# Optimization experiments

Measured on AMD Instinct MI355X. Metric: run time of the kernel, lower is better.

The kernel has to match this reference:

```python
import jax, jax.numpy as jnp
import numpy as np

B, S, H = 1, 1024, 2048
NH, NKV, HD = 32, 4, 128
E, K, I = 32, 8, 768
EPS = 1e-06
ROPE_BASE = 1e6


def rmsnorm(x, w, eps=EPS):
    xf = x.astype(jnp.float32)
    var = jnp.mean(xf * xf, axis=-1, keepdims=True)
    return w * (xf * jax.lax.rsqrt(var + eps)).astype(x.dtype)


def apply_rope(x, cos, sin):
    # x: [B,S,N,HD]; cos/sin: [S,HD//2]; interleaved (llama-style) pair rotation
    xr = x.reshape(*x.shape[:-1], HD // 2, 2)
    x0, x1 = xr[..., 0], xr[..., 1]
    c = cos[None, :, None, :]
    s = sin[None, :, None, :]
    o0 = x0 * c - x1 * s
    o1 = x0 * s + x1 * c
    return jnp.stack([o0, o1], axis=-1).reshape(x.shape)


def setup_inputs() -> dict:
    key = jax.random.key(0)
    ks = jax.random.split(key, 16)
    hidden_states = jax.random.normal(ks[0], (B, S, H), dtype=jnp.float32)
    # RoPE angles: positions * inv_freq  -> [S, HD//2]
    inv_freq = 1.0 / (ROPE_BASE ** (np.arange(0, HD, 2, dtype=np.float32) / HD))
    position_embeddings = jnp.asarray(np.arange(S, dtype=np.float32)[:, None] * inv_freq[None, :])
    # causal additive mask [1,1,S,S]
    causal = jnp.tril(jnp.ones((S, S), dtype=bool))
    attention_mask = jnp.where(causal, 0.0, -1e9).astype(jnp.float32)[None, None]
    w = 0.02
    params = {
        'ln1_w': jnp.ones((H,), jnp.float32),
        'ln2_w': jnp.ones((H,), jnp.float32),
        'q_w': w * jax.random.normal(ks[1], (H, NH * HD), jnp.float32),
        'k_w': w * jax.random.normal(ks[2], (H, NKV * HD), jnp.float32),
        'v_w': w * jax.random.normal(ks[3], (H, NKV * HD), jnp.float32),
        'o_w': w * jax.random.normal(ks[4], (NH * HD, H), jnp.float32),
        'qn_w': jnp.ones((HD,), jnp.float32),
        'kn_w': jnp.ones((HD,), jnp.float32),
        'gate_w': w * jax.random.normal(ks[5], (H, E), jnp.float32),
        'wg': w * jax.random.normal(ks[6], (E, H, I), jnp.float32),
        'wu': w * jax.random.normal(ks[7], (E, H, I), jnp.float32),
        'wd': w * jax.random.normal(ks[8], (E, I, H), jnp.float32),
    }
    return {'hidden_states': hidden_states, 'position_embeddings': position_embeddings,
            'attention_mask': attention_mask, 'start_pos': 0, **params}


def reference(hidden_states, position_embeddings, attention_mask, start_pos,
              ln1_w, ln2_w, q_w, k_w, v_w, o_w, qn_w, kn_w, gate_w, wg, wu, wd):
    x = hidden_states  # [B,S,H]
    # --- attention ---
    h = rmsnorm(x, ln1_w)
    q = rmsnorm((h @ q_w).reshape(B, S, NH, HD), qn_w)
    k = rmsnorm((h @ k_w).reshape(B, S, NKV, HD), kn_w)
    v = (h @ v_w).reshape(B, S, NKV, HD)
    cos, sin = jnp.cos(position_embeddings), jnp.sin(position_embeddings)
    q = apply_rope(q, cos, sin)
    k = apply_rope(k, cos, sin)
    q = q.transpose(0, 2, 1, 3)  # [B,NH,S,HD]
    k = jnp.repeat(k.transpose(0, 2, 1, 3), NH // NKV, axis=1)
    v = jnp.repeat(v.transpose(0, 2, 1, 3), NH // NKV, axis=1)
    scores = jnp.einsum('bhqd,bhkd->bhqk', q, k) * (HD ** -0.5) + attention_mask
    attn = jax.nn.softmax(scores, axis=-1)
    o = jnp.einsum('bhqk,bhkd->bhqd', attn, v).transpose(0, 2, 1, 3).reshape(B, S, NH * HD)
    x = x + o @ o_w
    # --- MoE ---
    h = rmsnorm(x, ln2_w).reshape(B * S, H)  # [T,H]
    probs = jax.nn.softmax((h @ gate_w).astype(jnp.float32), axis=-1)
    rw, sel = jax.lax.top_k(probs, K)  # [T,K]
    rw = rw / jnp.sum(rw, axis=-1, keepdims=True)  # norm_topk_prob
    T = B * S
    # dense combine weights [T,E]; zero for unselected experts (same math as loop)
    wte = jnp.zeros((T, E), jnp.float32).at[jnp.arange(T)[:, None], sel].add(rw).astype(h.dtype)
    g = jnp.einsum('th,ehi->tei', h, wg)
    u = jnp.einsum('th,ehi->tei', h, wu)
    act = jax.nn.silu(g) * u  # [T,E,I]
    moe = jnp.einsum('te,tei,eih->th', wte, act, wd)
    return x + moe.reshape(B, S, H)
```

## Files before the change

### kernel.cpp

```cpp
#include <hip/hip_runtime.h>
#include <hip/hip_bf16.h>

#define S_ 1024
#define H_ 2048
#define NH_ 32
#define NKV_ 4
#define HD_ 128
#define NE_ 32
#define TOPK_ 8
#define I_ 768
#define EPS_ 1e-6f
#define QS_ 5120
#define BK2 32
#define NPAR 4

typedef __bf16 bf16_t;
typedef __bf16 bf16x4v __attribute__((ext_vector_type(4)));
typedef __bf16 bf16x8 __attribute__((ext_vector_type(8)));
typedef float f32x4 __attribute__((ext_vector_type(4)));
typedef float f32x16 __attribute__((ext_vector_type(16)));
typedef unsigned short u16_t;
typedef unsigned int uint2v __attribute__((ext_vector_type(2)));
typedef unsigned int uint4v __attribute__((ext_vector_type(4)));

static __device__ __forceinline__ u16_t f2u(float x) {
  return __builtin_bit_cast(u16_t, (__bf16)x);
}
static __device__ __forceinline__ float u2f(u16_t u) {
  return (float)__builtin_bit_cast(__bf16, u);
}

static __device__ __forceinline__ void gload16(const bf16_t* g, bf16_t* l) {
  __builtin_amdgcn_global_load_lds(
      (const __attribute__((address_space(1))) unsigned int*)g,
      (__attribute__((address_space(3))) unsigned int*)l, 16, 0, 0);
}

static __device__ __forceinline__ int tile_lane_off(int lane) {
  return (lane >> 2) * 32 + (((lane & 3) ^ ((lane >> 3) & 3)) << 3);
}

template <bool WF32>
__global__ __launch_bounds__(256) void rmsnorm2_k(const float* __restrict__ x,
                                                  const float* __restrict__ w,
                                                  float* __restrict__ outf,
                                                  bf16_t* __restrict__ outb) {
  int r = blockIdx.x, tid = threadIdx.x;
  const float* xr = x + (size_t)r * H_;
  f32x4 a = *(const f32x4*)(xr + tid * 8);
  f32x4 b = *(const f32x4*)(xr + tid * 8 + 4);
  float ss = 0.f;
#pragma unroll
  for (int i = 0; i < 4; ++i) ss += a[i] * a[i] + b[i] * b[i];
#pragma unroll
  for (int m = 1; m < 64; m <<= 1) ss += __shfl_xor(ss, m);
  __shared__ float wsum[4];
  if ((tid & 63) == 0) wsum[tid >> 6] = ss;
  __syncthreads();
  ss = wsum[0] + wsum[1] + wsum[2] + wsum[3];
  float inv = rsqrtf(ss * (1.0f / H_) + EPS_);
  f32x4 w0 = *(const f32x4*)(w + tid * 8);
  f32x4 w1 = *(const f32x4*)(w + tid * 8 + 4);
  f32x4 o0, o1;
#pragma unroll
  for (int i = 0; i < 4; ++i) { o0[i] = a[i] * inv * w0[i]; o1[i] = b[i] * inv * w1[i]; }
  if constexpr (WF32) {
    *(f32x4*)(outf + (size_t)r * H_ + tid * 8) = o0;
    *(f32x4*)(outf + (size_t)r * H_ + tid * 8 + 4) = o1;
  }
  bf16x8 ob;
#pragma unroll
  for (int i = 0; i < 4; ++i) { ob[i] = (__bf16)o0[i]; ob[i + 4] = (__bf16)o1[i]; }
  *(bf16x8*)(outb + (size_t)r * H_ + tid * 8) = ob;
}

__global__ __launch_bounds__(256) void transp3_k(const float* __restrict__ in,
                                                 bf16_t* __restrict__ out, int R, int C) {
  __shared__ float tile[64][65];
  size_t z = (size_t)blockIdx.z * R * C;
  int tx = threadIdx.x & 15, ty = threadIdx.x >> 4;
  int r0 = blockIdx.y * 64, c0 = blockIdx.x * 64;
#pragma unroll
  for (int i = 0; i < 4; ++i) {
    f32x4 v = *(const f32x4*)(in + z + (size_t)(r0 + ty + i * 16) * C + c0 + tx * 4);
    tile[ty + i * 16][tx * 4 + 0] = v[0];
    tile[ty + i * 16][tx * 4 + 1] = v[1];
    tile[ty + i * 16][tx * 4 + 2] = v[2];
    tile[ty + i * 16][tx * 4 + 3] = v[3];
  }
  __syncthreads();
  int KT = R >> 5;
  int flat = threadIdx.x * 16;
  int lt = flat >> 9;
  int within = flat & 511;
  int nr = within >> 5;
  int kc = within & 31;
  int tn = lt >> 1, tk = lt & 1;
  bf16x8 o0, o1;
#pragma unroll
  for (int j = 0; j < 8; ++j) o0[j] = (bf16_t)tile[tk * 32 + kc + j][tn * 16 + nr];
#pragma unroll
  for (int j = 0; j < 8; ++j) o1[j] = (bf16_t)tile[tk * 32 + kc + 8 + j][tn * 16 + nr];
  size_t tidx = ((size_t)((c0 >> 4) + tn) * KT + (r0 >> 5) + tk) << 9;
  *(bf16x8*)(out + z + tidx + nr * 32 + kc) = o0;
  *(bf16x8*)(out + z + tidx + nr * 32 + kc + 8) = o1;
}

template <int BMT, int BNT, int WM, int WN, typename TC, bool RESID>
__global__ __launch_bounds__(512) void gemmd_k(
    const bf16_t* __restrict__ A, const bf16_t* __restrict__ Bt,
    const float* __restrict__ resid, TC* __restrict__ C, int M, int N, int K) {
  constexpr int MI = BMT / WM / 16;
  constexpr int NI = BNT / WN / 16;
  constexpr int ALW = BMT / 16 / 8;
  constexpr int NBL = BNT / 16;
  static_assert(NBL <= 8, "B wave loads");
  __shared__ __align__(16) bf16_t As[2][BMT][BK2];
  __shared__ __align__(16) bf16_t Bs[2][BNT][BK2];
  int tid = threadIdx.x, lane = tid & 63, w = tid >> 6;
  int m0 = blockIdx.x * BMT, n0 = blockIdx.y * BNT;
  int srow = lane >> 2;
  int schunk = ((lane & 3) ^ ((lane >> 3) & 3)) * 8;
  const bf16_t* asrc[ALW];
#pragma unroll
  for (int i = 0; i < ALW; ++i) {
    int r = (w * ALW + i) * 16 + srow;
    asrc[i] = A + (size_t)(m0 + r) * K + schunk;
  }
  bool hasB = (w < NBL);
  int brow = w * 16;
  const bf16_t* bsrc = nullptr;
  if (hasB)
    bsrc = Bt + ((size_t)((n0 + brow) >> 4) * (K >> 5)) * 512 + tile_lane_off(lane);

  int fr = lane & 15, g = lane >> 4;
  int rk = (g ^ ((fr >> 1) & 3)) * 8;
  int wm = w / WN, wn = w % WN;
  int rbase0 = wm * (BMT / WM), cbase0 = wn * (BNT / WN);
  f32x4 acc[MI][NI] = {};
  int NT = K / BK2;
  {
#pragma unroll
    for (int i = 0; i < ALW; ++i) gload16(asrc[i], &As[0][(w * ALW + i) * 16][0]);
    if (hasB) gload16(bsrc, &Bs[0][brow][0]);
  }
  __syncthreads();
  int cur = 0;
  for (int t = 0; t < NT; ++t) {
    if (t + 1 < NT) {
      int ko = (t + 1) * BK2;
#pragma unroll
      for (int i = 0; i < ALW; ++i) gload16(asrc[i] + ko, &As[cur ^ 1][(w * ALW + i) * 16][0]);
      if (hasB) gload16(bsrc + (size_t)(t + 1) * 512, &Bs[cur ^ 1][brow][0]);
    }
    bf16x8 af[MI], bf[NI];
#pragma unroll
    for (int i = 0; i < MI; ++i) af[i] = *(const bf16x8*)&As[cur][rbase0 + i * 16 + fr][rk];
#pragma unroll
    for (int i = 0; i < NI; ++i) bf[i] = *(const bf16x8*)&Bs[cur][cbase0 + i * 16 + fr][rk];
#pragma unroll
    for (int mi = 0; mi < MI; ++mi)
#pragma unroll
      for (int ni = 0; ni < NI; ++ni)
        acc[mi][ni] = __builtin_amdgcn_mfma_f32_16x16x32_bf16(af[mi], bf[ni], acc[mi][ni], 0, 0, 0);
    __syncthreads();
    cur ^= 1;
  }
  int rbase = g * 4;
#pragma unroll
  for (int mi = 0; mi < MI; ++mi)
#pragma unroll
    for (int ni = 0; ni < NI; ++ni)
#pragma unroll
      for (int r = 0; r < 4; ++r) {
        int gi = m0 + rbase0 + mi * 16 + rbase + r;
        int gc = n0 + cbase0 + ni * 16 + fr;
        float v = acc[mi][ni][r];
        if constexpr (RESID) v += resid[(size_t)gi * N + gc];
        C[(size_t)gi * N + gc] = (TC)v;
      }
}

template <int BNT, int WM, int WN, typename TC, bool GATHER, bool SCALE, bool DUAL>
__global__ __launch_bounds__(512) void gemme2_k(
    const bf16_t* __restrict__ A, const bf16_t* __restrict__ B1g,
    const bf16_t* __restrict__ B2g, TC* __restrict__ C, bf16_t* __restrict__ act,
    const float* __restrict__ wlist, const int* __restrict__ counts,
    const int* __restrict__ offsets, const int* __restrict__ toklist,
    const int* __restrict__ mslots, const int* __restrict__ meta,
    int* __restrict__ qhead, int NTN, int N, int K) {
  constexpr int BMT = 128;
  constexpr int MI = BMT / WM / 16;
  constexpr int NI = BNT / WN / 16;
  constexpr int BNTT = BNT * (DUAL ? 2 : 1);
  constexpr int NBT = BNTT / 16;
  constexpr int BPW = NBT / 8;
  static_assert(BPW * 8 == NBT, "B tile split");
  __shared__ __align__(16) bf16_t As[4][BMT][BK2];
  __shared__ __align__(16) bf16_t Bs[4][BNTT][BK2];
  __shared__ int s_w;
  int tid = threadIdx.x, lane = tid & 63, w = tid >> 6;
  int srow = lane >> 2;
  int schunk = ((lane & 3) ^ ((lane >> 3) & 3)) * 8;
  int tloff = tile_lane_off(lane);
  int fr = lane & 15, g = lane >> 4;
  int rk = (g ^ ((fr >> 1) & 3)) * 8;
  int wm = w / WN, wn = w % WN;
  int rbase0 = wm * (BMT / WM), cbase0 = wn * (BNT / WN);
  int KT = K >> 5;
  int SS = K >> 7;
  int total = meta[0] * NTN;
  for (;;) {
    if (tid == 0) s_w = atomicAdd(qhead, 1);
    __syncthreads();
    int wk = s_w;
    if (wk >= total) return;
    int ms = mslots[wk / NTN];
    int n0 = (wk % NTN) * BNT;
    int e = ms >> 8, m0 = (ms & 255) * BMT;
    int cnt = counts[e], off = offsets[e];
    size_t bs = (size_t)K * N;
    const bf16_t* B1 = B1g + (size_t)e * bs;
    const bf16_t* B2 = DUAL ? (B2g + (size_t)e * bs) : nullptr;
    const bf16_t* asrc;
    {
      int gr = min(m0 + w * 16 + srow, cnt - 1);
      size_t grow;
      if constexpr (GATHER) grow = (size_t)toklist[e * S_ + gr];
      else grow = (size_t)(off + gr);
      asrc = A + grow * (size_t)K + schunk;
    }
    const bf16_t* bsrc[BPW];
    int brow16[BPW];
#pragma unroll
    for (int j = 0; j < BPW; ++j) {
      int r16 = (w * BPW + j) * 16;
      brow16[j] = r16;
      const bf16_t* Bb = (r16 < BNT) ? B1 : B2;
      int rr = (r16 < BNT) ? r16 : r16 - BNT;
      bsrc[j] = Bb + ((size_t)((n0 + rr) >> 4) * KT) * 512 + tloff;
    }
    f32x4 acc1[MI][NI] = {};
    f32x4 acc2[DUAL ? MI : 1][DUAL ? NI : 1] = {};
    for (int ss = 0; ss < SS; ++ss) {
      int kbase = ss * 128;
#pragma unroll
      for (int sub = 0; sub < 4; ++sub)
        gload16(asrc + kbase + sub * BK2, &As[sub][w * 16][0]);
#pragma unroll
      for (int j = 0; j < BPW; ++j)
#pragma unroll
        for (int sub = 0; sub < 4; ++sub)
          gload16(bsrc[j] + (size_t)(ss * 4 + sub) * 512, &Bs[sub][brow16[j]][0]);
      __syncthreads();
#pragma unroll
      for (int sub = 0; sub < 4; ++sub) {
        bf16x8 af[MI], b1f[NI], b2f[DUAL ? NI : 1];
#pragma unroll
        for (int i = 0; i < MI; ++i) af[i] = *(const bf16x8*)&As[sub][rbase0 + i * 16 + fr][rk];
#pragma unroll
        for (int i = 0; i < NI; ++i) b1f[i] = *(const bf16x8*)&Bs[sub][cbase0 + i * 16 + fr][rk];
        if constexpr (DUAL) {
#pragma unroll
          for (int i = 0; i < NI; ++i) b2f[i] = *(const bf16x8*)&Bs[sub][BNT + cbase0 + i * 16 + fr][rk];
        }
#pragma unroll
        for (int mi = 0; mi < MI; ++mi)
#pragma unroll
          for (int ni = 0; ni < NI; ++ni) {
            acc1[mi][ni] = __builtin_amdgcn_mfma_f32_16x16x32_bf16(af[mi], b1f[ni], acc1[mi][ni], 0, 0, 0);
            if constexpr (DUAL)
              acc2[mi][ni] = __builtin_amdgcn_mfma_f32_16x16x32_bf16(af[mi], b2f[ni], acc2[mi][ni], 0, 0, 0);
          }
      }
      __syncthreads();
    }
    int rbase = g * 4;
#pragma unroll
    for (int mi = 0; mi < MI; ++mi)
#pragma unroll
      for (int ni = 0; ni < NI; ++ni)
#pragma unroll
        for (int r = 0; r < 4; ++r) {
          int lr = rbase0 + mi * 16 + rbase + r;
          int gi = m0 + lr;
          if (gi >= cnt) continue;
          int gc = n0 + cbase0 + ni * 16 + fr;
          if constexpr (DUAL) {
            float gv = acc1[mi][ni][r], uv = acc2[mi][ni][r];
            float sig = 1.0f / (1.0f + __expf(-gv));
            act[(size_t)(off + gi) * N + gc] = (bf16_t)(gv * sig * uv);
          } else {
            float v = acc1[mi][ni][r];
            if constexpr (SCALE) v *= wlist[(size_t)e * S_ + gi];
            C[(size_t)(off + gi) * N + gc] = (TC)v;
          }
        }
  }
}

__global__ __launch_bounds__(64) void qkpack_k(const float* __restrict__ qkv,
                                               const float* __restrict__ qn,
                                               const float* __restrict__ kn,
                                               const float* __restrict__ pe,
                                               bf16_t* __restrict__ Q2,
                                               bf16_t* __restrict__ K2) {
  int s = blockIdx.x, hh = blockIdx.y, lane = threadIdx.x;
  const float* ptr;
  const float* w;
  if (hh < NH_) { ptr = qkv + (size_t)s * QS_ + hh * HD_; w = qn; }
  else          { ptr = qkv + (size_t)s * QS_ + NH_ * HD_ + (hh - NH_) * HD_; w = kn; }
  float x0 = ptr[2 * lane], x1 = ptr[2 * lane + 1];
  float ss = x0 * x0 + x1 * x1;
#pragma unroll
  for (int m = 1; m < 64; m <<= 1) ss += __shfl_xor(ss, m);
  float inv = rsqrtf(ss * (1.0f / HD_) + EPS_);
  x0 = x0 * inv * w[2 * lane];
  x1 = x1 * inv * w[2 * lane + 1];
  float ang = pe[(size_t)s * (HD_ / 2) + lane];
  float sn, cs;
  sincosf(ang, &sn, &cs);
  float r0 = x0 * cs - x1 * sn;
  float r1 = x0 * sn + x1 * cs;
  if (hh < NH_) {
    const float scale = 0.08838834764831845f;
    float a = r0 * scale, b = r1 * scale;
    u16_t h0 = f2u(a), h1 = f2u(b);
    unsigned hw = (unsigned)h0 | ((unsigned)h1 << 16);
    unsigned lw = (unsigned)f2u(a - u2f(h0)) | ((unsigned)f2u(b - u2f(h1)) << 16);
    unsigned* base = (unsigned*)(Q2 + ((size_t)s * NH_ + hh) * 256);
    base[lane] = hw;
    base[64 + lane] = lw;
  } else {
    u16_t h0 = f2u(r0), h1 = f2u(r1);
    unsigned hw = (unsigned)h0 | ((unsigned)h1 << 16);
    unsigned lw = (unsigned)f2u(r0 - u2f(h0)) | ((unsigned)f2u(r1 - u2f(h1)) << 16);
    int j = lane >> 2, off = (2 * lane) & 7;
    unsigned* base = (unsigned*)(K2 + ((size_t)(hh - NH_) * S_ + s) * 256);
    base[(((j) ^ (s & 31)) * 8 + off) >> 1] = hw;
    base[(((16 + j) ^ (s & 31)) * 8 + off) >> 1] = lw;
  }
}

__global__ __launch_bounds__(256) void vpack_k(const float* __restrict__ qkv,
                                               bf16_t* __restrict__ V2T) {
  int t = blockIdx.x, kvh = blockIdx.y;
  int kv0 = t * 64;
  bf16_t* dst = V2T + (size_t)(kvh * 16 + t) * 128 * 128;
  const float* vbase = qkv + NH_ * HD_ + NKV_ * HD_ + kvh * HD_;
#pragma unroll
  for (int i = 0; i < 4; ++i) {
    int flat = threadIdx.x + i * 256;
    int kvp = flat >> 5, d4 = (flat & 31) * 4;
    const float* r0 = vbase + (size_t)(kv0 + 2 * kvp) * QS_ + d4;
    const float* r1 = r0 + QS_;
    f32x4 a = *(const f32x4*)r0;
    f32x4 b = *(const f32x4*)r1;
    int kvg = (2 * kvp) >> 3, sub = (2 * kvp) & 7;
#pragma unroll
    for (int e = 0; e < 4; ++e) {
      int d = d4 + e;
      int fsw = (d ^ (d >> 4)) & 15;
      u16_t ha = f2u(a[e]), hb = f2u(b[e]);
      unsigned hw = (unsigned)ha | ((unsigned)hb << 16);
      unsigned lw = (unsigned)f2u(a[e] - u2f(ha)) | ((unsigned)f2u(b[e] - u2f(hb)) << 16);
      unsigned* dd = (unsigned*)(dst + d * 128);
      dd[((kvg ^ fsw) * 8 + sub) >> 1] = hw;
      dd[(((8 + kvg) ^ fsw) * 8 + sub) >> 1] = lw;
    }
  }
}

#define AKV 64
__global__ __launch_bounds__(512, 4) void attn5_k(const bf16_t* __restrict__ Q2,
                                                  const bf16_t* __restrict__ K2,
                                                  const bf16_t* __restrict__ V2T,
                                                  float* __restrict__ Op,
                                                  float* __restrict__ mlp) {
  int q0 = blockIdx.x * 32;
  int kvh = blockIdx.y;
  int par = blockIdx.z;
  int tid = threadIdx.x, lane = tid & 63, w = tid >> 6;
  int g = lane >> 5, c32 = lane & 31;
  int h = kvh * 8 + w;
  int qrow = q0 + c32;
  int last_t = (q0 + 31) >> 6;
  float2* mlv = (float2*)mlp;
  if (par > last_t) {
    if (g == 0) {
      float2 v2; v2.x = -3.0e38f; v2.y = 0.f;
      mlv[((size_t)par * S_ + qrow) * NH_ + h] = v2;
    }
    return;
  }
  __shared__ __align__(16) u16_t Kl[AKV * 256];
  __shared__ __align__(16) u16_t Vl[128 * 128];

  bf16x8 qh[8], ql[8];
  {
    const bf16_t* qp2 = Q2 + ((size_t)qrow * NH_ + h) * 256;
#pragma unroll
    for (int ks = 0; ks < 8; ++ks) {
      qh[ks] = *(const bf16x8*)(qp2 + g * 8 + ks * 16);
      ql[ks] = *(const bf16x8*)(qp2 + 128 + g * 8 + ks * 16);
    }
  }

  f32x16 accO[4] = {};
  float m = -3.0e38f, l = 0.f;

  for (int t = par; t <= last_t; t += NPAR) {
    int kv0 = t * AKV;
    __syncthreads();
    {
      const bf16_t* ksrc = K2 + ((size_t)kvh * S_ + kv0) * 256;
#pragma unroll
      for (int i = 0; i < 4; ++i) {
        int cbase = w * 64 + i * 512;
        gload16(ksrc + (size_t)(cbase + lane) * 8, (bf16_t*)&Kl[cbase * 8]);
      }
    }
    {
      const bf16_t* vsrc = V2T + (size_t)(kvh * 16 + t) * 128 * 128;
#pragma unroll
      for (int i = 0; i < 4; ++i) {
        int cbase = w * 64 + i * 512;
        gload16(vsrc + (size_t)(cbase + lane) * 8, (bf16_t*)&Vl[cbase * 8]);
      }
    }
    __syncthreads();

    f32x16 accS[2] = {};
#pragma unroll
    for (int ks = 0; ks < 8; ++ks) {
      int db = g * 8 + ks * 16;
#pragma unroll
      for (int mf = 0; mf < 2; ++mf) {
        int kvr = c32 + mf * 32;
        bf16x8 ah = *(const bf16x8*)&Kl[kvr * 256 + (((db >> 3)) ^ c32) * 8];
        bf16x8 al = *(const bf16x8*)&Kl[kvr * 256 + ((16 + (db >> 3)) ^ c32) * 8];
        accS[mf] = __builtin_amdgcn_mfma_f32_32x32x16_bf16(ah, qh[ks], accS[mf], 0, 0, 0);
        accS[mf] = __builtin_amdgcn_mfma_f32_32x32x16_bf16(ah, ql[ks], accS[mf], 0, 0, 0);
        accS[mf] = __builtin_amdgcn_mfma_f32_32x32x16_bf16(al, qh[ks], accS[mf], 0, 0, 0);
      }
    }
    float p[2][16];
    float tmax = -3.0e38f;
#pragma unroll
    for (int mf = 0; mf < 2; ++mf)
#pragma unroll
      for (int r = 0; r < 16; ++r) {
        int kvg = kv0 + mf * 32 + (r & 3) + 8 * (r >> 2) + 4 * g;
        float s = (kvg <= qrow) ? accS[mf][r] : -3.0e38f;
        p[mf][r] = s;
        tmax = fmaxf(tmax, s);
      }
    tmax = fmaxf(tmax, __shfl_xor(tmax, 32));
    float mn = fmaxf(m, tmax);
    float sc = __expf(m - mn);
    float ts = 0.f;
#pragma unroll
    for (int mf = 0; mf < 2; ++mf)
#pragma unroll
      for (int r = 0; r < 16; ++r) {
        float e = __expf(p[mf][r] - mn);
        p[mf][r] = e;
        ts += e;
      }
    ts += __shfl_xor(ts, 32);
    l = l * sc + ts;
    m = mn;
#pragma unroll
    for (int r = 0; r < 16; ++r) {
      int row16 = (r & 3) + 8 * (r >> 2) + 4 * g;
      float scr = __shfl(sc, row16);
#pragma unroll
      for (int nf = 0; nf < 4; ++nf) accO[nf][r] *= scr;
    }
#pragma unroll
    for (int ks = 0; ks < 4; ++ks) {
      int k1 = ks & 1, mf = ks >> 1;
      unsigned Lh[4], Ll[4];
#pragma unroll
      for (int i = 0; i < 4; ++i) {
        float a = p[mf][8 * k1 + 2 * i], b = p[mf][8 * k1 + 2 * i + 1];
        u16_t ha = f2u(a), hb = f2u(b);
        Lh[i] = (unsigned)ha | ((unsigned)hb << 16);
        Ll[i] = (unsigned)f2u(a - u2f(ha)) | ((unsigned)f2u(b - u2f(hb)) << 16);
      }
      unsigned Xh[4], Xl[4];
#pragma unroll
      for (int i = 0; i < 4; ++i) {
        Xh[i] = (unsigned)__shfl_xor((int)Lh[i], 32);
        Xl[i] = (unsigned)__shfl_xor((int)Ll[i], 32);
      }
      uint4v fh, fl;
      fh[0] = g ? Xh[2] : Lh[0]; fh[1] = g ? Xh[3] : Lh[1];
      fh[2] = g ? Lh[2] : Xh[0]; fh[3] = g ? Lh[3] : Xh[1];
      fl[0] = g ? Xl[2] : Ll[0]; fl[1] = g ? Xl[3] : Ll[1];
      fl[2] = g ? Ll[2] : Xl[0]; fl[3] = g ? Ll[3] : Xl[1];
      bf16x8 pH = __builtin_bit_cast(bf16x8, fh);
      bf16x8 pL = __builtin_bit_cast(bf16x8, fl);
      int kvb = g * 8 + ks * 16;
#pragma unroll
      for (int nf = 0; nf < 4; ++nf) {
        int d = c32 + nf * 32;
        int fsw = (d ^ (d >> 4)) & 15;
        bf16x8 vh = *(const bf16x8*)&Vl[d * 128 + (((kvb >> 3)) ^ fsw) * 8];
        bf16x8 vl = *(const bf16x8*)&Vl[d * 128 + ((8 + (kvb >> 3)) ^ fsw) * 8];
        accO[nf] = __builtin_amdgcn_mfma_f32_32x32x16_bf16(pH, vh, accO[nf], 0, 0, 0);
        accO[nf] = __builtin_amdgcn_mfma_f32_32x32x16_bf16(pH, vl, accO[nf], 0, 0, 0);
        accO[nf] = __builtin_amdgcn_mfma_f32_32x32x16_bf16(pL, vh, accO[nf], 0, 0, 0);
      }
    }
  }
#pragma unroll
  for (int r = 0; r < 16; ++r) {
    int row16 = (r & 3) + 8 * (r >> 2) + 4 * g;
    int orow = q0 + row16;
#pragma unroll
    for (int nf = 0; nf < 4; ++nf)
      __builtin_nontemporal_store(
          accO[nf][r], &Op[(((size_t)par * S_ + orow) * NH_ + h) * HD_ + nf * 32 + c32]);
  }
  if (g == 0) {
    float2 v2; v2.x = m; v2.y = l;
    mlv[((size_t)par * S_ + qrow) * NH_ + h] = v2;
  }
}

__global__ __launch_bounds__(128) void attnmerge_k(const float* __restrict__ Op,
                                                   const float* __restrict__ mlp,
                                                   bf16_t* __restrict__ o) {
  int row = blockIdx.x, h = blockIdx.y, d = threadIdx.x;
  const float2* mlv = (const float2*)mlp;
  float mm[NPAR], ll[NPAR];
  float M = -3.0e38f;
#pragma unroll
  for (int p = 0; p < NPAR; ++p) {
    float2 v2 = mlv[((size_t)p * S_ + row) * NH_ + h];
    mm[p] = v2.x; ll[p] = v2.y;
    M = fmaxf(M, mm[p]);
  }
  float acc = 0.f, L = 0.f;
#pragma unroll
  for (int p = 0; p < NPAR; ++p) {
    if (ll[p] == 0.f) continue;
    float wp = __expf(mm[p] - M);
    acc += wp * __builtin_nontemporal_load(
                    &Op[(((size_t)p * S_ + row) * NH_ + h) * HD_ + d]);
    L += wp * ll[p];
  }
  o[((size_t)row * NH_ + h) * HD_ + d] = (bf16_t)(acc / L);
}

__global__ __launch_bounds__(256) void router2_k(const float* __restrict__ h2,
                                                 const float* __restrict__ gw,
                                                 int* __restrict__ sel,
                                                 float* __restrict__ wsel) {
  int t = blockIdx.x, tid = threadIdx.x;
  int e = tid & 31, grp = tid >> 5;
  float acc = 0.f;
  for (int kk = grp; kk < H_; kk += 8)
    acc += h2[(size_t)t * H_ + kk] * gw[(size_t)kk * NE_ + e];
  __shared__ float part[8][32];
  part[grp][e] = acc;
  __syncthreads();
  if (tid < 64) {
    int lane = tid;
    float lg = -3.0e38f;
    if (lane < 32) {
      lg = 0.f;
      for (int g = 0; g < 8; ++g) lg += part[g][lane];
    }
    float tm = lg;
#pragma unroll
    for (int mm = 1; mm < 32; mm <<= 1) tm = fmaxf(tm, __shfl_xor(tm, mm));
    if (lane < 32) lg = __expf(lg - tm);
    bool avail = (lane < 32);
    float tot = 0.f;
    int se[TOPK_]; float rw[TOPK_];
#pragma unroll
    for (int kk = 0; kk < TOPK_; ++kk) {
      float val = avail ? lg : -1.f;
      float best = val;
#pragma unroll
      for (int mm = 1; mm < 32; mm <<= 1) best = fmaxf(best, __shfl_xor(best, mm));
      unsigned long long ball = __ballot(avail && (val == best));
      int bi = (int)__builtin_ctzll(ball);
      if (lane == bi) avail = false;
      se[kk] = bi;
      rw[kk] = best;
      tot += best;
    }
    float itot = 1.0f / tot;
    if (lane == 0) {
#pragma unroll
      for (int kk = 0; kk < TOPK_; ++kk) {
        sel[t * TOPK_ + kk] = se[kk];
        wsel[t * TOPK_ + kk] = rw[kk] * itot;
      }
    }
  }
}

__global__ __launch_bounds__(64) void build_k(const int* __restrict__ sel,
                                              const float* __restrict__ wsel,
                                              int* __restrict__ counts,
                                              int* __restrict__ toklist,
                                              float* __restrict__ wlist,
                                              int* __restrict__ pos) {
  int e = blockIdx.x, lane = threadIdx.x;
  int base = 0;
  for (int c = 0; c < S_ / 64; ++c) {
    int t = c * 64 + lane;
    int match = -1;
#pragma unroll
    for (int k = 0; k < TOPK_; ++k)
      if (sel[t * TOPK_ + k] == e) match = k;
    bool flag = (match >= 0);
    unsigned long long mask = __ballot(flag);
    int prefix = __popcll(mask & ((1ull << lane) - 1ull));
    if (flag) {
      int p = base + prefix;
      toklist[e * S_ + p] = t;
      wlist[e * S_ + p] = wsel[t * TOPK_ + match];
      pos[t * TOPK_ + match] = p;
    }
    base += __popcll(mask);
  }
  if (lane == 0) counts[e] = base;
}

__global__ void scan_k(const int* __restrict__ counts, int* __restrict__ offsets,
                       int* __restrict__ mslots, int* __restrict__ meta,
                       int* __restrict__ qheads) {
  if (threadIdx.x == 0 && blockIdx.x == 0) {
    int o = 0, ns = 0;
    for (int e = 0; e < NE_; ++e) {
      offsets[e] = o;
      int c = counts[e];
      for (int m0 = 0; m0 < c; m0 += 128) mslots[ns++] = (e << 8) | (m0 >> 7);
      o += c;
    }
    offsets[NE_] = o;
    meta[0] = ns;
    qheads[0] = 0;
    qheads[1] = 0;
  }
}

__global__ __launch_bounds__(256) void combine_k(const float* __restrict__ x1,
                                                 const bf16_t* __restrict__ pairout,
                                                 const int* __restrict__ sel,
                                                 const int* __restrict__ pos,
                                                 const int* __restrict__ offsets,
                                                 float* __restrict__ out) {
  int t = blockIdx.x, tid = threadIdx.x;
  int slots[TOPK_];
#pragma unroll
  for (int kk = 0; kk < TOPK_; ++kk)
    slots[kk] = offsets[sel[t * TOPK_ + kk]] + pos[t * TOPK_ + kk];
  int c = tid * 8;
  f32x4 s0 = *(const f32x4*)(x1 + (size_t)t * H_ + c);
  f32x4 s1 = *(const f32x4*)(x1 + (size_t)t * H_ + c + 4);
#pragma unroll
  for (int kk = 0; kk < TOPK_; ++kk) {
    bf16x8 pv = *(const bf16x8*)(pairout + (size_t)slots[kk] * H_ + c);
#pragma unroll
    for (int i = 0; i < 4; ++i) { s0[i] += (float)pv[i]; s1[i] += (float)pv[i + 4]; }
  }
  *(f32x4*)(out + (size_t)t * H_ + c) = s0;
  *(f32x4*)(out + (size_t)t * H_ + c + 4) = s1;
}

extern "C" void kernel_launch(void* const* d_in, const int* in_sizes, int n_in,
                              void* d_out, int out_size, void* d_ws, size_t ws_size,
                              hipStream_t stream) {
  const float* hidden = (const float*)d_in[0];
  const float* pe     = (const float*)d_in[1];
  const float* ln1    = (const float*)d_in[4];
  const float* ln2    = (const float*)d_in[5];
  const float* q_w    = (const float*)d_in[6];
  const float* k_w    = (const float*)d_in[7];
  const float* v_w    = (const float*)d_in[8];
  const float* o_w    = (const float*)d_in[9];
  const float* qn     = (const float*)d_in[10];
  const float* kn     = (const float*)d_in[11];
  const float* gate_w = (const float*)d_in[12];
  const float* wg     = (const float*)d_in[13];
  const float* wu     = (const float*)d_in[14];
  const float* wd     = (const float*)d_in[15];
  float* out = (float*)d_out;

  char* p = (char*)d_ws;
  auto alloc = [&](size_t bytes) {
    char* r = p;
    p += (bytes + 255) & ~(size_t)255;
    return r;
  };
  bf16_t* h1b     = (bf16_t*)alloc((size_t)S_ * H_ * 2);
  float*  qkv     = (float*)alloc((size_t)S_ * QS_ * 4);
  bf16_t* Q2      = (bf16_t*)alloc((size_t)S_ * NH_ * 256 * 2);
  bf16_t* K2      = (bf16_t*)alloc((size_t)NKV_ * S_ * 256 * 2);
  bf16_t* V2T     = (bf16_t*)alloc((size_t)NKV_ * 16 * 128 * 128 * 2);
  bf16_t* aob     = (bf16_t*)alloc((size_t)S_ * NH_ * HD_ * 2);
  float*  x1      = (float*)alloc((size_t)S_ * H_ * 4);
  float*  h2      = (float*)alloc((size_t)S_ * H_ * 4);
  bf16_t* h2b     = (bf16_t*)alloc((size_t)S_ * H_ * 2);
  bf16_t* act     = (bf16_t*)alloc((size_t)S_ * TOPK_ * I_ * 2);
  bf16_t* po      = (bf16_t*)alloc((size_t)S_ * TOPK_ * H_ * 2);
  float*  Opart   = (float*)alloc((size_t)NPAR * S_ * NH_ * HD_ * 4);
  float*  mlpart  = (float*)alloc((size_t)NPAR * S_ * NH_ * 8);
  int*    counts  = (int*)alloc(NE_ * 4);
  int*    offs    = (int*)alloc((NE_ + 1) * 4);
  int*    toklist = (int*)alloc((size_t)NE_ * S_ * 4);
  float*  wlist   = (float*)alloc((size_t)NE_ * S_ * 4);
  int*    sel     = (int*)alloc((size_t)S_ * TOPK_ * 4);
  float*  wsel    = (float*)alloc((size_t)S_ * TOPK_ * 4);
  int*    pos     = (int*)alloc((size_t)S_ * TOPK_ * 4);
  int*    mslots  = (int*)alloc(512 * 4);
  int*    meta    = (int*)alloc(4);
  int*    qheads  = (int*)alloc(2 * 4);
  bf16_t* qkvT = (bf16_t*)alloc((size_t)QS_ * H_ * 2);
  bf16_t* owT  = (bf16_t*)alloc((size_t)(NH_ * HD_) * H_ * 2);
  bf16_t* wgT  = (bf16_t*)alloc((size_t)NE_ * H_ * I_ * 2);
  bf16_t* wuT  = (bf16_t*)alloc((size_t)NE_ * H_ * I_ * 2);
  bf16_t* wdT  = (bf16_t*)alloc((size_t)NE_ * I_ * H_ * 2);
  bf16_t* qwTp = qkvT;
  bf16_t* kwTp = qkvT + (size_t)(NH_ * HD_) * H_;
  bf16_t* vwTp = qkvT + (size_t)(NH_ * HD_ + NKV_ * HD_) * H_;

  transp3_k<<<dim3((NH_ * HD_) / 64, H_ / 64, 1), 256, 0, stream>>>(q_w, qwTp, H_, NH_ * HD_);
  transp3_k<<<dim3((NKV_ * HD_) / 64, H_ / 64, 1), 256, 0, stream>>>(k_w, kwTp, H_, NKV_ * HD_);
  transp3_k<<<dim3((NKV_ * HD_) / 64, H_ / 64, 1), 256, 0, stream>>>(v_w, vwTp, H_, NKV_ * HD_);
  transp3_k<<<dim3(H_ / 64, (NH_ * HD_) / 64, 1), 256, 0, stream>>>(o_w, owT, NH_ * HD_, H_);
  transp3_k<<<dim3(I_ / 64, H_ / 64, NE_), 256, 0, stream>>>(wg, wgT, H_, I_);
  transp3_k<<<dim3(I_ / 64, H_ / 64, NE_), 256, 0, stream>>>(wu, wuT, H_, I_);
  transp3_k<<<dim3(H_ / 64, I_ / 64, NE_), 256, 0, stream>>>(wd, wdT, I_, H_);

  rmsnorm2_k<false><<<S_, 256, 0, stream>>>(hidden, ln1, nullptr, h1b);
  gemmd_k<256, 128, 4, 2, float, false>
      <<<dim3(S_ / 256, QS_ / 128), 512, 0, stream>>>(h1b, qkvT, nullptr, qkv, S_, QS_, H_);
  qkpack_k<<<dim3(S_, NH_ + NKV_), 64, 0, stream>>>(qkv, qn, kn, pe, Q2, K2);
  vpack_k<<<dim3(16, NKV_), 256, 0, stream>>>(qkv, V2T);
  attn5_k<<<dim3(S_ / 32, NKV_, NPAR), 512, 0, stream>>>(Q2, K2, V2T, Opart, mlpart);
  attnmerge_k<<<dim3(S_, NH_), 128, 0, stream>>>(Opart, mlpart, aob);
  gemmd_k<128, 64, 4, 2, float, true>
      <<<dim3(S_ / 128, H_ / 64), 512, 0, stream>>>(aob, owT, hidden, x1, S_, H_, NH_ * HD_);
  rmsnorm2_k<true><<<S_, 256, 0, stream>>>(x1, ln2, h2, h2b);
  router2_k<<<S_, 256, 0, stream>>>(h2, gate_w, sel, wsel);
  build_k<<<NE_, 64, 0, stream>>>(sel, wsel, counts, toklist, wlist, pos);
  scan_k<<<1, 64, 0, stream>>>(counts, offs, mslots, meta, qheads);
  gemme2_k<128, 2, 4, float, true, false, true>
      <<<256, 512, 0, stream>>>(h2b, wgT, wuT, nullptr, act, wlist, counts, offs, toklist,
                                mslots, meta, &qheads[0], I_ / 128, I_, H_);
  gemme2_k<256, 2, 4, bf16_t, false, true, false>
      <<<256, 512, 0, stream>>>(act, wdT, nullptr, po, nullptr, wlist, counts, offs, nullptr,
                                mslots, meta, &qheads[1], H_ / 256, H_, I_);
  combine_k<<<S_, 256, 0, stream>>>(x1, po, sel, pos, offs, out);
}
```

Baseline: 830.2 us.

## Drop split-KV attention and merge kernel; normalize output in-kernel

Removes the 4-way KV split of the attention kernel and the separate merge kernel. Each block now walks all causal KV tiles itself, divides by the softmax sum in registers and writes bf16 output directly. This saves the fp32 partial-output round trip through memory and one kernel launch. In exchange the grid shrinks fourfold (128 blocks), so there is less parallelism and the causal work is spread less evenly across blocks.

```diff
diff --git a/kernel.cpp b/kernel.cpp
--- a/kernel.cpp
+++ b/kernel.cpp
@@ -12,7 +12,6 @@
 #define EPS_ 1e-6f
 #define QS_ 5120
 #define BK2 32
-#define NPAR 4
 
 typedef __bf16 bf16_t;
 typedef __bf16 bf16x4v __attribute__((ext_vector_type(4)));
@@ -372,27 +371,17 @@
 }
 
 #define AKV 64
-__global__ __launch_bounds__(512, 4) void attn5_k(const bf16_t* __restrict__ Q2,
+__global__ __launch_bounds__(512, 2) void attn6_k(const bf16_t* __restrict__ Q2,
                                                   const bf16_t* __restrict__ K2,
                                                   const bf16_t* __restrict__ V2T,
-                                                  float* __restrict__ Op,
-                                                  float* __restrict__ mlp) {
+                                                  bf16_t* __restrict__ o) {
   int q0 = blockIdx.x * 32;
   int kvh = blockIdx.y;
-  int par = blockIdx.z;
   int tid = threadIdx.x, lane = tid & 63, w = tid >> 6;
   int g = lane >> 5, c32 = lane & 31;
   int h = kvh * 8 + w;
   int qrow = q0 + c32;
   int last_t = (q0 + 31) >> 6;
-  float2* mlv = (float2*)mlp;
-  if (par > last_t) {
-    if (g == 0) {
-      float2 v2; v2.x = -3.0e38f; v2.y = 0.f;
-      mlv[((size_t)par * S_ + qrow) * NH_ + h] = v2;
-    }
-    return;
-  }
   __shared__ __align__(16) u16_t Kl[AKV * 256];
   __shared__ __align__(16) u16_t Vl[128 * 128];
 
@@ -409,7 +398,7 @@
   f32x16 accO[4] = {};
   float m = -3.0e38f, l = 0.f;
 
-  for (int t = par; t <= last_t; t += NPAR) {
+  for (int t = 0; t <= last_t; ++t) {
     int kv0 = t * AKV;
     __syncthreads();
     {
@@ -514,44 +503,16 @@
       }
     }
   }
+  float invl = 1.0f / l;
 #pragma unroll
   for (int r = 0; r < 16; ++r) {
     int row16 = (r & 3) + 8 * (r >> 2) + 4 * g;
+    float il = __shfl(invl, row16);
     int orow = q0 + row16;
 #pragma unroll
     for (int nf = 0; nf < 4; ++nf)
-      __builtin_nontemporal_store(
-          accO[nf][r], &Op[(((size_t)par * S_ + orow) * NH_ + h) * HD_ + nf * 32 + c32]);
-  }
-  if (g == 0) {
-    float2 v2; v2.x = m; v2.y = l;
-    mlv[((size_t)par * S_ + qrow) * NH_ + h] = v2;
-  }
-}
-
-__global__ __launch_bounds__(128) void attnmerge_k(const float* __restrict__ Op,
-                                                   const float* __restrict__ mlp,
-                                                   bf16_t* __restrict__ o) {
-  int row = blockIdx.x, h = blockIdx.y, d = threadIdx.x;
-  const float2* mlv = (const float2*)mlp;
-  float mm[NPAR], ll[NPAR];
-  float M = -3.0e38f;
-#pragma unroll
-  for (int p = 0; p < NPAR; ++p) {
-    float2 v2 = mlv[((size_t)p * S_ + row) * NH_ + h];
-    mm[p] = v2.x; ll[p] = v2.y;
-    M = fmaxf(M, mm[p]);
-  }
-  float acc = 0.f, L = 0.f;
-#pragma unroll
-  for (int p = 0; p < NPAR; ++p) {
-    if (ll[p] == 0.f) continue;
-    float wp = __expf(mm[p] - M);
-    acc += wp * __builtin_nontemporal_load(
-                    &Op[(((size_t)p * S_ + row) * NH_ + h) * HD_ + d]);
-    L += wp * ll[p];
-  }
-  o[((size_t)row * NH_ + h) * HD_ + d] = (bf16_t)(acc / L);
+      o[((size_t)orow * NH_ + h) * HD_ + nf * 32 + c32] = (bf16_t)(accO[nf][r] * il);
+  }
 }
 
 __global__ __launch_bounds__(256) void router2_k(const float* __restrict__ h2,
@@ -710,8 +671,6 @@
   bf16_t* h2b     = (bf16_t*)alloc((size_t)S_ * H_ * 2);
   bf16_t* act     = (bf16_t*)alloc((size_t)S_ * TOPK_ * I_ * 2);
   bf16_t* po      = (bf16_t*)alloc((size_t)S_ * TOPK_ * H_ * 2);
-  float*  Opart   = (float*)alloc((size_t)NPAR * S_ * NH_ * HD_ * 4);
-  float*  mlpart  = (float*)alloc((size_t)NPAR * S_ * NH_ * 8);
   int*    counts  = (int*)alloc(NE_ * 4);
   int*    offs    = (int*)alloc((NE_ + 1) * 4);
   int*    toklist = (int*)alloc((size_t)NE_ * S_ * 4);
@@ -744,8 +703,7 @@
       <<<dim3(S_ / 256, QS_ / 128), 512, 0, stream>>>(h1b, qkvT, nullptr, qkv, S_, QS_, H_);
   qkpack_k<<<dim3(S_, NH_ + NKV_), 64, 0, stream>>>(qkv, qn, kn, pe, Q2, K2);
   vpack_k<<<dim3(16, NKV_), 256, 0, stream>>>(qkv, V2T);
-  attn5_k<<<dim3(S_ / 32, NKV_, NPAR), 512, 0, stream>>>(Q2, K2, V2T, Opart, mlpart);
-  attnmerge_k<<<dim3(S_, NH_), 128, 0, stream>>>(Opart, mlpart, aob);
+  attn6_k<<<dim3(S_ / 32, NKV_), 512, 0, stream>>>(Q2, K2, V2T, aob);
   gemmd_k<128, 64, 4, 2, float, true>
       <<<dim3(S_ / 128, H_ / 64), 512, 0, stream>>>(aob, owT, hidden, x1, S_, H_, NH_ * HD_);
   rmsnorm2_k<true><<<S_, 256, 0, stream>>>(x1, ln2, h2, h2b);
```

After: 782.5 us. 5.8% less time.
